# Optimization experiments

Hardware: AMD Instinct MI355X
Metric: run time of the kernel (lower is better)

## Reference

```python
import jax, jax.numpy as jnp
import numpy as np

DIM = 1024
HEADS = 16
DIM_HEAD = 64
DEPTH = 12
LN_EPS = 1e-5


def setup_inputs() -> dict:
    key = jax.random.key(0)
    k1, k2, k3 = jax.random.split(key, 3)
    B, N = 4, 2048
    inner = HEADS * DIM_HEAD
    x = jax.random.normal(k1, (B, N, DIM), dtype=jnp.float32)
    ln_w = jnp.ones((DIM,), jnp.float32)
    ln_b = jnp.zeros((DIM,), jnp.float32)
    w_qkv = jax.random.normal(k2, (DIM, 3 * inner), jnp.float32) * (DIM ** -0.5)
    w_out = jax.random.normal(k3, (inner, DIM), jnp.float32) * (inner ** -0.5)
    b_out = jnp.zeros((DIM,), jnp.float32)
    return {"x": x, "ln_w": ln_w, "ln_b": ln_b, "w_qkv": w_qkv,
            "w_out": w_out, "b_out": b_out, "layer_index": 2}


def reference(x, ln_w, ln_b, w_qkv, w_out, b_out, layer_index):
    B, N, D = x.shape
    scale = DIM_HEAD ** -0.5
    # LayerNorm
    mu = jnp.mean(x, axis=-1, keepdims=True)
    var = jnp.mean(jnp.square(x - mu), axis=-1, keepdims=True)
    xn = (x - mu) * jax.lax.rsqrt(var + LN_EPS) * ln_w + ln_b
    # QKV projection (no bias), split heads: b n (h d) -> b h n d
    qkv = xn @ w_qkv  # [B, N, 3*H*Dh]
    q, k, v = jnp.split(qkv, 3, axis=-1)
    def heads(t):
        return t.reshape(B, N, HEADS, DIM_HEAD).transpose(0, 2, 1, 3)
    q, k, v = heads(q), heads(k), heads(v)
    dots = jnp.einsum('bhnd,bhmd->bhnm', q, k) * scale  # [B,H,N,N]
    if layer_index < DEPTH // 2:
        attn = jax.nn.relu(dots)
    else:
        attn = jax.nn.softmax(dots, axis=-1)
    attn = attn / N  # divide by x.shape[1]
    out = jnp.einsum('bhnm,bhmd->bhnd', attn, v)
    out = out.transpose(0, 2, 1, 3).reshape(B, N, HEADS * DIM_HEAD)
    # to_out (heads > 1): Linear + (inactive) dropout
    return out @ w_out + b_out
```

## Files before the change

### kernel.cpp

```cpp
#include <hip/hip_runtime.h>
#include <stdint.h>

typedef __bf16 bf16x8 __attribute__((ext_vector_type(8)));
typedef __bf16 bf16x4 __attribute__((ext_vector_type(4)));
typedef float f32x4 __attribute__((ext_vector_type(4)));

#define PSCALE (0.125f / 2048.0f)

#define GLOAD16(src, dst)                                                      \
  __builtin_amdgcn_global_load_lds(                                            \
      (__attribute__((address_space(1))) void*)const_cast<__bf16*>(src),       \
      (__attribute__((address_space(3))) void*)(dst), 16, 0, 0)

__global__ __launch_bounds__(256) void ln_fused(const float* __restrict__ x,
                                                const float* __restrict__ w,
                                                const float* __restrict__ b,
                                                __bf16* __restrict__ xn) {
  const int row = blockIdx.x;
  const int t = threadIdx.x;
  const float4 v = ((const float4*)(x + (size_t)row * 1024))[t];
  float s = v.x + v.y + v.z + v.w;
  float ss = v.x * v.x + v.y * v.y + v.z * v.z + v.w * v.w;
#pragma unroll
  for (int o = 32; o; o >>= 1) {
    s += __shfl_down(s, o);
    ss += __shfl_down(ss, o);
  }
  __shared__ float red[8];
  if ((t & 63) == 0) {
    red[t >> 6] = s;
    red[4 + (t >> 6)] = ss;
  }
  __syncthreads();
  const float tot = red[0] + red[1] + red[2] + red[3];
  const float tot2 = red[4] + red[5] + red[6] + red[7];
  const float mu = tot * (1.0f / 1024.0f);
  const float var = tot2 * (1.0f / 1024.0f) - mu * mu;
  const float rs = rsqrtf(var + 1e-5f);
  const float4 wv = ((const float4*)w)[t];
  const float4 bv = ((const float4*)b)[t];
  bf16x4 o;
  o[0] = (__bf16)((v.x - mu) * rs * wv.x + bv.x);
  o[1] = (__bf16)((v.y - mu) * rs * wv.y + bv.y);
  o[2] = (__bf16)((v.z - mu) * rs * wv.z + bv.z);
  o[3] = (__bf16)((v.w - mu) * rs * wv.w + bv.w);
  ((bf16x4*)xn)[(size_t)row * 256 + t] = o;
}

__global__ __launch_bounds__(256) void transpose_cvt(const float* __restrict__ A,
                                                     __bf16* __restrict__ At,
                                                     int R, int C) {
  __shared__ __bf16 T[64][72];
  const int rb = blockIdx.y * 64, cb = blockIdx.x * 64;
  const int tid = threadIdx.x;
  const int r = tid >> 2, cg = tid & 3;
#pragma unroll
  for (int k = 0; k < 4; ++k) {
    const float4 v =
        *(const float4*)(A + (size_t)(rb + r) * C + cb + cg * 16 + k * 4);
    T[cg * 16 + k * 4 + 0][r] = (__bf16)v.x;
    T[cg * 16 + k * 4 + 1][r] = (__bf16)v.y;
    T[cg * 16 + k * 4 + 2][r] = (__bf16)v.z;
    T[cg * 16 + k * 4 + 3][r] = (__bf16)v.w;
  }
  __syncthreads();
#pragma unroll
  for (int i = 0; i < 2; ++i) {
    const int j = i * 256 + tid;
    const int c = j >> 3, s8 = j & 7;
    const bf16x8 o = *(const bf16x8*)&T[c][s8 * 8];
    *(bf16x8*)(At + (size_t)(cb + c) * R + rb + s8 * 8) = o;
  }
}

template <int MODE>
__global__ __launch_bounds__(512) void gemm_nt(
    const __bf16* __restrict__ A, const __bf16* __restrict__ B, int K,
    float* __restrict__ outF, __bf16* __restrict__ Qo, __bf16* __restrict__ Ko,
    __bf16* __restrict__ Vto, const float* __restrict__ bias) {
  __shared__ __bf16 Sm[3 * 24576];
  const int tid = threadIdx.x;
  const int lane = tid & 63, w = tid >> 6;
  const int g = lane >> 4, c15 = lane & 15;
  const int wr = w >> 2, wc = w & 3;
  const int rb = blockIdx.y * 128, cb = blockIdx.x * 256;

  const __bf16* aSp[2];
  const __bf16* bSp[4];
  int aDo[2], bDo[4];
#pragma unroll
  for (int i = 0; i < 2; ++i) {
    const int j = i * 512 + tid, row = j >> 3, slot = j & 7;
    aSp[i] = A + (size_t)(rb + row) * K + ((slot ^ (row & 7)) << 3);
    aDo[i] = i * 4096 + w * 512;
  }
#pragma unroll
  for (int i = 0; i < 4; ++i) {
    const int j = i * 512 + tid, col = j >> 3, slot = j & 7;
    bSp[i] = B + (size_t)(cb + col) * K + ((slot ^ (col & 7)) << 3);
    bDo[i] = 8192 + i * 4096 + w * 512;
  }

  f32x4 acc[4][4] = {};
  const int nkb = K >> 6;

#pragma unroll
  for (int t = 0; t < 2; ++t) {
    __bf16* dst = Sm + t * 24576;
#pragma unroll
    for (int i = 0; i < 2; ++i) GLOAD16(aSp[i] + t * 64, dst + aDo[i]);
#pragma unroll
    for (int i = 0; i < 4; ++i) GLOAD16(bSp[i] + t * 64, dst + bDo[i]);
  }

  int cur = 0, stg = 2, koff = 128;
  for (int kb = 0; kb < nkb; ++kb) {
    if (kb == nkb - 1) {
      asm volatile("s_waitcnt vmcnt(0)" ::: "memory");
    } else {
      asm volatile("s_waitcnt vmcnt(6)" ::: "memory");
    }
    __builtin_amdgcn_s_barrier();
    if (kb < nkb - 2) {
      __bf16* dst = Sm + stg * 24576;
#pragma unroll
      for (int i = 0; i < 2; ++i) GLOAD16(aSp[i] + koff, dst + aDo[i]);
#pragma unroll
      for (int i = 0; i < 4; ++i) GLOAD16(bSp[i] + koff, dst + bDo[i]);
      koff += 64;
    }
    const __bf16* __restrict__ Ac = Sm + cur * 24576;
    const __bf16* __restrict__ Bc = Ac + 8192;
#pragma unroll
    for (int ks = 0; ks < 2; ++ks) {
      bf16x8 af[4], bfr[4];
      const int kc = ks * 4 + g;
#pragma unroll
      for (int rt = 0; rt < 4; ++rt) {
        const int lr = wr * 64 + rt * 16 + c15;
        af[rt] = *(const bf16x8*)(Ac + lr * 64 + ((kc ^ (lr & 7)) << 3));
      }
#pragma unroll
      for (int ct = 0; ct < 4; ++ct) {
        const int lc = wc * 64 + ct * 16 + c15;
        bfr[ct] = *(const bf16x8*)(Bc + lc * 64 + ((kc ^ (lc & 7)) << 3));
      }
      __builtin_amdgcn_s_setprio(1);
#pragma unroll
      for (int rt = 0; rt < 4; ++rt)
#pragma unroll
        for (int ct = 0; ct < 4; ++ct)
          acc[rt][ct] = __builtin_amdgcn_mfma_f32_16x16x32_bf16(
              af[rt], bfr[ct], acc[rt][ct], 0, 0, 0);
      __builtin_amdgcn_s_setprio(0);
    }
    cur = (cur == 2) ? 0 : cur + 1;
    stg = (stg == 2) ? 0 : stg + 1;
  }
  const int r00 = rb + wr * 64 + g * 4;
  if (MODE == 1) {
#pragma unroll
    for (int ct = 0; ct < 4; ++ct) {
      const int col = cb + wc * 64 + ct * 16 + c15;
      const float bv = bias[col];
#pragma unroll
      for (int rt = 0; rt < 4; ++rt) {
        const int row = r00 + rt * 16;
#pragma unroll
        for (int r = 0; r < 4; ++r)
          outF[(size_t)(row + r) * 1024 + col] = acc[rt][ct][r] + bv;
      }
    }
  } else {
#pragma unroll
    for (int ct = 0; ct < 4; ++ct) {
      const int col = cb + wc * 64 + ct * 16 + c15;
      const int part = col >> 10, rem = col & 1023;
      const int h = rem >> 6, d = rem & 63;
#pragma unroll
      for (int rt = 0; rt < 4; ++rt) {
        const int row = r00 + rt * 16;
        const int bi = row >> 11, n = row & 2047;
        const size_t bh = (size_t)bi * 16 + h;
        if (part == 2) {
          bf16x4 pv;
#pragma unroll
          for (int r = 0; r < 4; ++r) pv[r] = (__bf16)acc[rt][ct][r];
          *(bf16x4*)(Vto + (bh * 64 + d) * 2048 + n) = pv;
        } else if (part == 0) {
          __bf16* dst = Qo + (bh * 2048 + n) * 64 + d;
#pragma unroll
          for (int r = 0; r < 4; ++r)
            dst[(size_t)r * 64] = (__bf16)(acc[rt][ct][r] * PSCALE);
        } else {
          __bf16* dst = Ko + (bh * 2048 + n) * 64 + d;
#pragma unroll
          for (int r = 0; r < 4; ++r) dst[(size_t)r * 64] = (__bf16)acc[rt][ct][r];
        }
      }
    }
  }
}

__global__ __launch_bounds__(512) void attn_relu(
    const __bf16* __restrict__ Q, const __bf16* __restrict__ K,
    const __bf16* __restrict__ Vt, __bf16* __restrict__ O) {
  __shared__ __bf16 Ks[2][128 * 64];
  __shared__ __bf16 Vs[2][64 * 128];
  const int tid = threadIdx.x;
  const int lane = tid & 63, w = tid >> 6;
  const int g = lane >> 4, c15 = lane & 15;
  const int bh = blockIdx.x, qb = blockIdx.y;
  const __bf16* Qg = Q + ((size_t)bh * 2048 + qb * 256) * 64;
  const __bf16* Kg = K + (size_t)bh * 2048 * 64;
  const __bf16* Vg = Vt + (size_t)bh * 64 * 2048;

  const __bf16* kp0;
  const __bf16* kp1;
  const __bf16* vp0;
  const __bf16* vp1;
  {
    const int j0 = tid, j1 = 512 + tid;
    const int r0_ = j0 >> 3, s0_ = j0 & 7;
    const int r1_ = j1 >> 3, s1_ = j1 & 7;
    const int sr0 = (r0_ & 96) | ((r0_ & 12) << 1) | ((r0_ & 16) >> 2) | (r0_ & 3);
    const int sr1 = (r1_ & 96) | ((r1_ & 12) << 1) | ((r1_ & 16) >> 2) | (r1_ & 3);
    kp0 = Kg + (size_t)sr0 * 64 + ((s0_ ^ (r0_ & 7)) << 3);
    kp1 = Kg + (size_t)sr1 * 64 + ((s1_ ^ (r1_ & 7)) << 3);
    const int d0_ = j0 >> 4, t0_ = j0 & 15;
    const int d1_ = j1 >> 4, t1_ = j1 & 15;
    vp0 = Vg + (size_t)d0_ * 2048 + ((t0_ ^ (d0_ & 15)) << 3);
    vp1 = Vg + (size_t)d1_ * 2048 + ((t1_ ^ (d1_ & 15)) << 3);
  }
  const int dstoff = w * 64 * 8;

  bf16x8 qf[2][2];
#pragma unroll
  for (int rt = 0; rt < 2; ++rt)
#pragma unroll
    for (int ks = 0; ks < 2; ++ks) {
      const int row = w * 32 + rt * 16 + c15;
      qf[rt][ks] = *(const bf16x8*)(Qg + row * 64 + ks * 32 + (g << 3));
    }
  f32x4 oacc[2][4] = {};

  GLOAD16(kp0, Ks[0] + dstoff);
  GLOAD16(kp1, Ks[0] + 512 * 8 + dstoff);
  GLOAD16(vp0, Vs[0] + dstoff);
  GLOAD16(vp1, Vs[0] + 512 * 8 + dstoff);
  kp0 += 128 * 64; kp1 += 128 * 64; vp0 += 128; vp1 += 128;

  for (int kb = 0; kb < 16; ++kb) {
    const int cur = kb & 1;
    if (kb < 15) {
      GLOAD16(kp0, Ks[cur ^ 1] + dstoff);
      GLOAD16(kp1, Ks[cur ^ 1] + 512 * 8 + dstoff);
      GLOAD16(vp0, Vs[cur ^ 1] + dstoff);
      GLOAD16(vp1, Vs[cur ^ 1] + 512 * 8 + dstoff);
      kp0 += 128 * 64; kp1 += 128 * 64; vp0 += 128; vp1 += 128;
      asm volatile("s_waitcnt vmcnt(4)" ::: "memory");
    } else {
      asm volatile("s_waitcnt vmcnt(0)" ::: "memory");
    }
    __builtin_amdgcn_s_barrier();
    const __bf16* __restrict__ Kc = Ks[cur];
    const __bf16* __restrict__ Vc = Vs[cur];
#pragma unroll
    for (int u = 0; u < 4; ++u) {
      const int kra = u * 32 + c15;
      const int krb = u * 32 + 16 + c15;
      const bf16x8 kfa0 = *(const bf16x8*)(Kc + kra * 64 + ((g ^ (kra & 7)) << 3));
      const bf16x8 kfa1 = *(const bf16x8*)(Kc + kra * 64 + (((4 + g) ^ (kra & 7)) << 3));
      const bf16x8 kfb0 = *(const bf16x8*)(Kc + krb * 64 + ((g ^ (krb & 7)) << 3));
      const bf16x8 kfb1 = *(const bf16x8*)(Kc + krb * 64 + (((4 + g) ^ (krb & 7)) << 3));
      f32x4 sa[2] = {{}, {}}, sb[2] = {{}, {}};
      __builtin_amdgcn_s_setprio(1);
#pragma unroll
      for (int rt = 0; rt < 2; ++rt) {
        sa[rt] = __builtin_amdgcn_mfma_f32_16x16x32_bf16(kfa0, qf[rt][0], sa[rt], 0, 0, 0);
        sa[rt] = __builtin_amdgcn_mfma_f32_16x16x32_bf16(kfa1, qf[rt][1], sa[rt], 0, 0, 0);
        sb[rt] = __builtin_amdgcn_mfma_f32_16x16x32_bf16(kfb0, qf[rt][0], sb[rt], 0, 0, 0);
        sb[rt] = __builtin_amdgcn_mfma_f32_16x16x32_bf16(kfb1, qf[rt][1], sb[rt], 0, 0, 0);
      }
      __builtin_amdgcn_s_setprio(0);
      bf16x8 pa[2];
#pragma unroll
      for (int rt = 0; rt < 2; ++rt)
#pragma unroll
        for (int r = 0; r < 4; ++r) {
          pa[rt][r] = (__bf16)fmaxf(sa[rt][r], 0.0f);
          pa[rt][4 + r] = (__bf16)fmaxf(sb[rt][r], 0.0f);
        }
      __builtin_amdgcn_s_setprio(1);
#pragma unroll
      for (int dt = 0; dt < 4; ++dt) {
        const int d = dt * 16 + c15;
        const bf16x8 vb = *(const bf16x8*)(Vc + d * 128 + (((4 * u + g) ^ c15) << 3));
#pragma unroll
        for (int rt = 0; rt < 2; ++rt)
          oacc[rt][dt] = __builtin_amdgcn_mfma_f32_16x16x32_bf16(
              pa[rt], vb, oacc[rt][dt], 0, 0, 0);
      }
      __builtin_amdgcn_s_setprio(0);
    }
    __builtin_amdgcn_s_barrier();
  }
  const int bi = bh >> 4, h = bh & 15;
#pragma unroll
  for (int rt = 0; rt < 2; ++rt)
#pragma unroll
    for (int dt = 0; dt < 4; ++dt) {
      const int col = h * 64 + dt * 16 + c15;
      const int n0 = qb * 256 + w * 32 + rt * 16 + g * 4;
      __bf16* dst = O + ((size_t)bi * 2048 + n0) * 1024 + col;
#pragma unroll
      for (int r = 0; r < 4; ++r) dst[(size_t)r * 1024] = (__bf16)oacc[rt][dt][r];
    }
}

extern "C" void kernel_launch(void* const* d_in, const int* in_sizes, int n_in,
                              void* d_out, int out_size, void* d_ws,
                              size_t ws_size, hipStream_t stream) {
  (void)in_sizes; (void)n_in; (void)out_size; (void)ws_size;
  const float* x = (const float*)d_in[0];
  const float* ln_w = (const float*)d_in[1];
  const float* ln_b = (const float*)d_in[2];
  const float* w_qkv = (const float*)d_in[3];
  const float* w_out = (const float*)d_in[4];
  const float* b_out = (const float*)d_in[5];
  char* ws = (char*)d_ws;
  __bf16* xn = (__bf16*)(ws);
  __bf16* Wt1 = (__bf16*)(ws + (size_t)(16u << 20));
  __bf16* Wt2 = (__bf16*)(ws + (size_t)(22u << 20));
  __bf16* Qb = (__bf16*)(ws + (size_t)(24u << 20));
  __bf16* Kb = (__bf16*)(ws + (size_t)(40u << 20));
  __bf16* Vtb = (__bf16*)(ws + (size_t)(56u << 20));
  __bf16* Ob = (__bf16*)(ws + (size_t)(72u << 20));
  float* out = (float*)d_out;

  ln_fused<<<8192, 256, 0, stream>>>(x, ln_w, ln_b, xn);
  transpose_cvt<<<dim3(48, 16), 256, 0, stream>>>(w_qkv, Wt1, 1024, 3072);
  transpose_cvt<<<dim3(16, 16), 256, 0, stream>>>(w_out, Wt2, 1024, 1024);
  gemm_nt<0><<<dim3(12, 64), 512, 0, stream>>>(xn, Wt1, 1024, nullptr, Qb, Kb,
                                               Vtb, nullptr);
  attn_relu<<<dim3(64, 8), 512, 0, stream>>>(Qb, Kb, Vtb, Ob);
  gemm_nt<1><<<dim3(4, 64), 512, 0, stream>>>(Ob, Wt2, 1024, out, nullptr,
                                              nullptr, nullptr, b_out);
}
```

Before: 165.9 us.

## Merge prep kernels, remap GEMM blocks across XCDs, split stage loads around MFMA

Folds the LayerNorm kernel and the two weight transpose-convert kernels into a single prep launch that picks its role from the block index. This removes two kernel launches and their gaps. The GEMM now remaps its linear block index so that consecutive tiles land in contiguous chunks per XCD, aiming for better L2 locality. The GEMM main loop also issues the A-tile prefetch before the first k-substep and the B-tile prefetch between the two substeps, spreading global-to-LDS traffic across MFMA work. The remap assumes the grid size is divisible by 8.

```diff
diff --git a/kernel.cpp b/kernel.cpp
--- a/kernel.cpp
+++ b/kernel.cpp
@@ -12,48 +12,58 @@
       (__attribute__((address_space(1))) void*)const_cast<__bf16*>(src),       \
       (__attribute__((address_space(3))) void*)(dst), 16, 0, 0)
 
-__global__ __launch_bounds__(256) void ln_fused(const float* __restrict__ x,
-                                                const float* __restrict__ w,
-                                                const float* __restrict__ b,
-                                                __bf16* __restrict__ xn) {
-  const int row = blockIdx.x;
+__global__ __launch_bounds__(256) void prep(
+    const float* __restrict__ x, const float* __restrict__ lw,
+    const float* __restrict__ lb, __bf16* __restrict__ xn,
+    const float* __restrict__ w_qkv, __bf16* __restrict__ Wt1,
+    const float* __restrict__ w_out, __bf16* __restrict__ Wt2) {
+  __shared__ __bf16 T[64][72];
+  __shared__ float red[8];
+  const int b = blockIdx.x;
   const int t = threadIdx.x;
-  const float4 v = ((const float4*)(x + (size_t)row * 1024))[t];
-  float s = v.x + v.y + v.z + v.w;
-  float ss = v.x * v.x + v.y * v.y + v.z * v.z + v.w * v.w;
-#pragma unroll
-  for (int o = 32; o; o >>= 1) {
-    s += __shfl_down(s, o);
-    ss += __shfl_down(ss, o);
-  }
-  __shared__ float red[8];
-  if ((t & 63) == 0) {
-    red[t >> 6] = s;
-    red[4 + (t >> 6)] = ss;
-  }
-  __syncthreads();
-  const float tot = red[0] + red[1] + red[2] + red[3];
-  const float tot2 = red[4] + red[5] + red[6] + red[7];
-  const float mu = tot * (1.0f / 1024.0f);
-  const float var = tot2 * (1.0f / 1024.0f) - mu * mu;
-  const float rs = rsqrtf(var + 1e-5f);
-  const float4 wv = ((const float4*)w)[t];
-  const float4 bv = ((const float4*)b)[t];
-  bf16x4 o;
-  o[0] = (__bf16)((v.x - mu) * rs * wv.x + bv.x);
-  o[1] = (__bf16)((v.y - mu) * rs * wv.y + bv.y);
-  o[2] = (__bf16)((v.z - mu) * rs * wv.z + bv.z);
-  o[3] = (__bf16)((v.w - mu) * rs * wv.w + bv.w);
-  ((bf16x4*)xn)[(size_t)row * 256 + t] = o;
-}
-
-__global__ __launch_bounds__(256) void transpose_cvt(const float* __restrict__ A,
-                                                     __bf16* __restrict__ At,
-                                                     int R, int C) {
-  __shared__ __bf16 T[64][72];
-  const int rb = blockIdx.y * 64, cb = blockIdx.x * 64;
-  const int tid = threadIdx.x;
-  const int r = tid >> 2, cg = tid & 3;
+  if (b < 8192) {
+    const float4 v = ((const float4*)(x + (size_t)b * 1024))[t];
+    float s = v.x + v.y + v.z + v.w;
+    float ss = v.x * v.x + v.y * v.y + v.z * v.z + v.w * v.w;
+#pragma unroll
+    for (int o = 32; o; o >>= 1) {
+      s += __shfl_down(s, o);
+      ss += __shfl_down(ss, o);
+    }
+    if ((t & 63) == 0) {
+      red[t >> 6] = s;
+      red[4 + (t >> 6)] = ss;
+    }
+    __syncthreads();
+    const float tot = red[0] + red[1] + red[2] + red[3];
+    const float tot2 = red[4] + red[5] + red[6] + red[7];
+    const float mu = tot * (1.0f / 1024.0f);
+    const float var = tot2 * (1.0f / 1024.0f) - mu * mu;
+    const float rs = rsqrtf(var + 1e-5f);
+    const float4 wv = ((const float4*)lw)[t];
+    const float4 bv = ((const float4*)lb)[t];
+    bf16x4 o;
+    o[0] = (__bf16)((v.x - mu) * rs * wv.x + bv.x);
+    o[1] = (__bf16)((v.y - mu) * rs * wv.y + bv.y);
+    o[2] = (__bf16)((v.z - mu) * rs * wv.z + bv.z);
+    o[3] = (__bf16)((v.w - mu) * rs * wv.w + bv.w);
+    ((bf16x4*)xn)[(size_t)b * 256 + t] = o;
+    return;
+  }
+  const float* A;
+  __bf16* At;
+  int R, C, bx, by;
+  if (b < 8960) {
+    const int ti = b - 8192;
+    A = w_qkv; At = Wt1; R = 1024; C = 3072;
+    bx = ti % 48; by = ti / 48;
+  } else {
+    const int ti = b - 8960;
+    A = w_out; At = Wt2; R = 1024; C = 1024;
+    bx = ti % 16; by = ti / 16;
+  }
+  const int rb = by * 64, cb = bx * 64;
+  const int r = t >> 2, cg = t & 3;
 #pragma unroll
   for (int k = 0; k < 4; ++k) {
     const float4 v =
@@ -66,7 +76,7 @@
   __syncthreads();
 #pragma unroll
   for (int i = 0; i < 2; ++i) {
-    const int j = i * 256 + tid;
+    const int j = i * 256 + t;
     const int c = j >> 3, s8 = j & 7;
     const bf16x8 o = *(const bf16x8*)&T[c][s8 * 8];
     *(bf16x8*)(At + (size_t)(cb + c) * R + rb + s8 * 8) = o;
@@ -83,7 +93,10 @@
   const int lane = tid & 63, w = tid >> 6;
   const int g = lane >> 4, c15 = lane & 15;
   const int wr = w >> 2, wc = w & 3;
-  const int rb = blockIdx.y * 128, cb = blockIdx.x * 256;
+  const int linear = blockIdx.y * gridDim.x + blockIdx.x;
+  const int per = (gridDim.x * gridDim.y) >> 3;
+  const int nl = (linear & 7) * per + (linear >> 3);
+  const int rb = (nl / gridDim.x) * 128, cb = (nl % gridDim.x) * 256;
 
   const __bf16* aSp[2];
   const __bf16* bSp[4];
@@ -121,20 +134,44 @@
       asm volatile("s_waitcnt vmcnt(6)" ::: "memory");
     }
     __builtin_amdgcn_s_barrier();
-    if (kb < nkb - 2) {
-      __bf16* dst = Sm + stg * 24576;
-#pragma unroll
-      for (int i = 0; i < 2; ++i) GLOAD16(aSp[i] + koff, dst + aDo[i]);
-#pragma unroll
-      for (int i = 0; i < 4; ++i) GLOAD16(bSp[i] + koff, dst + bDo[i]);
-      koff += 64;
+    const bool do_stage = (kb < nkb - 2);
+    __bf16* sdst = Sm + stg * 24576;
+    if (do_stage) {
+#pragma unroll
+      for (int i = 0; i < 2; ++i) GLOAD16(aSp[i] + koff, sdst + aDo[i]);
     }
     const __bf16* __restrict__ Ac = Sm + cur * 24576;
     const __bf16* __restrict__ Bc = Ac + 8192;
-#pragma unroll
-    for (int ks = 0; ks < 2; ++ks) {
+    {
       bf16x8 af[4], bfr[4];
-      const int kc = ks * 4 + g;
+      const int kc = g;
+#pragma unroll
+      for (int rt = 0; rt < 4; ++rt) {
+        const int lr = wr * 64 + rt * 16 + c15;
+        af[rt] = *(const bf16x8*)(Ac + lr * 64 + ((kc ^ (lr & 7)) << 3));
+      }
+#pragma unroll
+      for (int ct = 0; ct < 4; ++ct) {
+        const int lc = wc * 64 + ct * 16 + c15;
+        bfr[ct] = *(const bf16x8*)(Bc + lc * 64 + ((kc ^ (lc & 7)) << 3));
+      }
+      __builtin_amdgcn_s_setprio(1);
+#pragma unroll
+      for (int rt = 0; rt < 4; ++rt)
+#pragma unroll
+        for (int ct = 0; ct < 4; ++ct)
+          acc[rt][ct] = __builtin_amdgcn_mfma_f32_16x16x32_bf16(
+              af[rt], bfr[ct], acc[rt][ct], 0, 0, 0);
+      __builtin_amdgcn_s_setprio(0);
+    }
+    if (do_stage) {
+#pragma unroll
+      for (int i = 0; i < 4; ++i) GLOAD16(bSp[i] + koff, sdst + bDo[i]);
+      koff += 64;
+    }
+    {
+      bf16x8 af[4], bfr[4];
+      const int kc = 4 + g;
 #pragma unroll
       for (int rt = 0; rt < 4; ++rt) {
         const int lr = wr * 64 + rt * 16 + c15;
@@ -338,9 +375,7 @@
   __bf16* Ob = (__bf16*)(ws + (size_t)(72u << 20));
   float* out = (float*)d_out;
 
-  ln_fused<<<8192, 256, 0, stream>>>(x, ln_w, ln_b, xn);
-  transpose_cvt<<<dim3(48, 16), 256, 0, stream>>>(w_qkv, Wt1, 1024, 3072);
-  transpose_cvt<<<dim3(16, 16), 256, 0, stream>>>(w_out, Wt2, 1024, 1024);
+  prep<<<9216, 256, 0, stream>>>(x, ln_w, ln_b, xn, w_qkv, Wt1, w_out, Wt2);
   gemm_nt<0><<<dim3(12, 64), 512, 0, stream>>>(xn, Wt1, 1024, nullptr, Qb, Kb,
                                                Vtb, nullptr);
   attn_relu<<<dim3(64, 8), 512, 0, stream>>>(Qb, Kb, Vtb, Ob);
```

New measurement: 159.4 us. 3.9% less time.
